# Performance work log

Hardware: AMD Instinct MI355X
Metric: run time of the kernel (lower is better)

## Reference

```python
import jax, jax.numpy as jnp
import numpy as np

N = 100000   # nodes
E = 3200000  # edges (avg degree 32)
F = 10       # input features
H = 20       # hidden dim
G = 512      # graphs in batch
L = 2        # labels


def xavier(key, shape):
    fan_in, fan_out = shape[0], shape[1]
    a = jnp.sqrt(6.0 / (fan_in + fan_out))
    return jax.random.uniform(key, shape, jnp.float32, -a, a)


def setup_inputs() -> dict:
    key = jax.random.key(0)
    ks = jax.random.split(key, 12)
    x = jax.random.normal(ks[0], (N, F), jnp.float32)
    edge_index = jax.random.randint(ks[1], (2, E), 0, N, jnp.int64)
    batch = jnp.sort(jax.random.randint(ks[2], (N,), 0, G, jnp.int64))
    return {
        "x": x,
        "edge_index": edge_index,
        "batch": batch,
        # layer 1: F -> H
        "W_rel1": xavier(ks[3], (F, H)), "b1": jnp.zeros((H,), jnp.float32),
        "W_root1": xavier(ks[4], (F, H)),
        # layer 2: H -> H
        "W_rel2": xavier(ks[5], (H, H)), "b2": jnp.zeros((H,), jnp.float32),
        "W_root2": xavier(ks[6], (H, H)),
        # layer 3: H -> H
        "W_rel3": xavier(ks[7], (H, H)), "b3": jnp.zeros((H,), jnp.float32),
        "W_root3": xavier(ks[8], (H, H)),
        # readout linear: 2H -> L
        "W_lin": xavier(ks[9], (2 * H, L)), "b_lin": jnp.zeros((L,), jnp.float32),
    }


def _graph_conv(x, src, dst, W_rel, b, W_root):
    # PyG GraphConv: out = lin_rel(sum_{j->i} x_j) + lin_root(x_i)
    agg = jax.ops.segment_sum(x[src], dst, num_segments=N)  # [N, d_in]
    return agg @ W_rel + b + x @ W_root


def reference(x, edge_index, batch, W_rel1, b1, W_root1, W_rel2, b2, W_root2,
              W_rel3, b3, W_root3, W_lin, b_lin):
    src, dst = edge_index[0], edge_index[1]
    h = jax.nn.relu(_graph_conv(x, src, dst, W_rel1, b1, W_root1))
    h = jax.nn.relu(_graph_conv(h, src, dst, W_rel2, b2, W_root2))
    h = jax.nn.relu(_graph_conv(h, src, dst, W_rel3, b3, W_root3))  # [N, H]
    # global max / mean pool over graphs
    maxp = jax.ops.segment_max(h, batch, num_segments=G)            # [G, H]
    sump = jax.ops.segment_sum(h, batch, num_segments=G)            # [G, H]
    counts = jax.ops.segment_sum(jnp.ones((h.shape[0], 1), h.dtype), batch,
                                 num_segments=G)                    # [G, 1]
    nonempty = counts > 0
    maxp = jnp.where(nonempty, maxp, 0.0)
    meanp = sump / jnp.maximum(counts, 1.0)
    pooled = jnp.concatenate([maxp, meanp], axis=-1)                # [G, 2H]
    return pooled @ W_lin + b_lin
```

## Files before the change

kernel.cpp:

```cpp
#include <hip/hip_runtime.h>
#include <hip/hip_bf16.h>

#define NN 100000
#define FF 10
#define HH 20
#define GG 512
#define LL 2

#define NB 500
#define BNODES 200
#define CAP 7168
#define HB 100
#define SCAP 3712
#define TILE 4096
#define SRC_BITS 17
#define SRC_MASK 0x1FFFFu

__device__ inline unsigned short f2bf(float f) {
  unsigned u = __float_as_uint(f);
  unsigned r = u + 0x7FFFu + ((u >> 16) & 1u);
  return (unsigned short)(r >> 16);
}
__device__ inline float bflo(unsigned u) { return __uint_as_float(u << 16); }
__device__ inline float bfhi(unsigned u) { return __uint_as_float(u & 0xFFFF0000u); }

__global__ __launch_bounds__(512) void init_kernel(
    float* __restrict__ sump, int* __restrict__ maxp, float* __restrict__ cnt,
    int* __restrict__ cursor) {
  int i = blockIdx.x * 512 + threadIdx.x;
  if (i < GG * HH) {
    sump[i] = 0.0f;
    maxp[i] = 0;
  }
  if (i < GG) cnt[i] = 0.0f;
  if (i < NB) cursor[i] = 0;
}

__global__ __launch_bounds__(512) void multisplit_kernel(
    const int* __restrict__ src, const int* __restrict__ dst,
    int* __restrict__ cursor, unsigned int* __restrict__ pay, int E,
    const float* __restrict__ x, unsigned short* __restrict__ xb, int ncast) {
  __shared__ int lhist[NB];
  __shared__ int lofs[NB];
  __shared__ int gbase[NB];
  __shared__ int lcur[NB];
  __shared__ unsigned int sord[TILE];
  __shared__ unsigned short sdbk[TILE];
  __shared__ int ss[512];
  int t = threadIdx.x;

  {
    int per = (ncast + gridDim.x - 1) / gridDim.x;
    int c0 = blockIdx.x * per;
    int c1 = c0 + per;
    if (c1 > ncast) c1 = ncast;
    for (int i = c0 + t; i < c1; i += 512)
      xb[i] = f2bf(__builtin_nontemporal_load(x + i));
  }

  if (t < NB) lhist[t] = 0;
  __syncthreads();

  int base = blockIdx.x * TILE;
  int count = E - base;
  if (count > TILE) count = TILE;

  for (int i = t; i < count; i += 512)
    atomicAdd(&lhist[dst[base + i] / BNODES], 1);
  __syncthreads();

  int own = (t < NB) ? lhist[t] : 0;
  ss[t] = own;
  __syncthreads();
  for (int off = 1; off < 512; off <<= 1) {
    int a0 = (t >= off) ? ss[t - off] : 0;
    __syncthreads();
    ss[t] += a0;
    __syncthreads();
  }
  if (t < NB) {
    lofs[t] = ss[t] - own;
    int bo = own ? atomicAdd(&cursor[t], own) : 0;
    if (bo > CAP - own) bo = CAP - own;
    gbase[t] = t * CAP + bo;
    lcur[t] = 0;
  }
  __syncthreads();

  for (int i = t; i < count; i += 512) {
    int e = base + i;
    int d = __builtin_nontemporal_load(dst + e);
    int s = __builtin_nontemporal_load(src + e);
    int bk = d / BNODES;
    int ld = d - bk * BNODES;
    int r = atomicAdd(&lcur[bk], 1);
    int slot = lofs[bk] + r;
    sord[slot] = ((unsigned)ld << SRC_BITS) | (unsigned)s;
    sdbk[slot] = (unsigned short)bk;
  }
  __syncthreads();

  for (int i = t; i < count; i += 512) {
    int bk = sdbk[i];
    pay[gbase[bk] + (i - lofs[bk])] = sord[i];
  }
}

__global__ __launch_bounds__(512) void bucket_csr_kernel(
    const unsigned int* __restrict__ pay, const int* __restrict__ cursor,
    int* __restrict__ srt, int* __restrict__ rofs, int* __restrict__ rend) {
  __shared__ int lhist[BNODES];
  __shared__ int lofs[BNODES];
  __shared__ int lcur[BNODES];
  __shared__ int ss[512];
  int b = blockIdx.x;
  int t = threadIdx.x;
  int k0 = b * CAP;
  int ecnt = cursor[b];
  if (ecnt > CAP) ecnt = CAP;

  if (t < BNODES) lhist[t] = 0;
  __syncthreads();
  for (int k = t; k < ecnt; k += 512)
    atomicAdd(&lhist[pay[k0 + k] >> SRC_BITS], 1);
  __syncthreads();

  int own = (t < BNODES) ? lhist[t] : 0;
  ss[t] = own;
  __syncthreads();
  for (int off = 1; off < 512; off <<= 1) {
    int a0 = (t >= off) ? ss[t - off] : 0;
    __syncthreads();
    ss[t] += a0;
    __syncthreads();
  }
  if (t < BNODES) {
    int ex = ss[t] - own;
    lofs[t] = ex;
    lcur[t] = 0;
    rofs[b * BNODES + t] = k0 + ex;
    rend[b * BNODES + t] = k0 + ex + own;
  }
  __syncthreads();

  for (int k = t; k < ecnt; k += 512) {
    unsigned p = pay[k0 + k];
    int ld = p >> SRC_BITS;
    int r = atomicAdd(&lcur[ld], 1);
    srt[k0 + lofs[ld] + r] = (int)(p & SRC_MASK);
  }
}

template<int DIN>
__global__ __launch_bounds__(512) void bucket_layer_kernel(
    const unsigned short* __restrict__ hin, const int* __restrict__ srt,
    const int* __restrict__ rofs, const int* __restrict__ rend,
    const float* __restrict__ Wrel, const float* __restrict__ bias,
    const float* __restrict__ Wroot, unsigned short* __restrict__ hout) {
  constexpr int AST = (DIN == 10) ? 11 : 21;
  constexpr int CH = DIN / 5;
  __shared__ int sSrc[SCAP];
  __shared__ float acc[HB * AST];
  __shared__ unsigned short roots[HB * DIN];
  __shared__ float sWrel[DIN * HH];
  __shared__ float sWroot[DIN * HH];
  __shared__ float sb[HH];
  __shared__ int sRofs[HB];
  __shared__ int sRend[HB];
  __shared__ int sSeg0, sSegLen;
  int b2 = blockIdx.x;
  int t = threadIdx.x;
  int nbase = b2 * HB;

  for (int i = t; i < DIN * HH; i += 512) {
    sWrel[i] = Wrel[i];
    sWroot[i] = Wroot[i];
  }
  if (t < HH) sb[t] = bias[t];
  if (t < HB) {
    sRofs[t] = rofs[nbase + t];
    sRend[t] = rend[nbase + t];
  }
  if (t == 0) {
    int s0 = rofs[nbase];
    int sl = rend[nbase + HB - 1] - s0;
    sSeg0 = s0;
    sSegLen = sl < SCAP ? sl : SCAP;
  }
  {
    const unsigned* rs = (const unsigned*)(hin + (size_t)nbase * DIN);
    unsigned* rd = (unsigned*)roots;
    for (int i = t; i < HB * DIN / 2; i += 512) rd[i] = rs[i];
  }
  __syncthreads();

  int seg0 = sSeg0, seglen = sSegLen;
  for (int i = t; i < seglen; i += 512)
    sSrc[i] = __builtin_nontemporal_load(srt + seg0 + i);
  __syncthreads();

  if (t < HB * 5) {
    int ln = t / 5;
    int c = t - ln * 5;
    int k0 = sRofs[ln] - seg0;
    int k1 = sRend[ln] - seg0;
    if (k1 > seglen) k1 = seglen;
    const unsigned short* xb = hin + c * CH;
    if (CH == 4) {
      float a0 = 0, a1 = 0, a2 = 0, a3 = 0;
      float b0 = 0, b1 = 0, b2 = 0, b3 = 0;
      int k = k0;
      for (; k + 3 < k1; k += 4) {
        int s0 = sSrc[k], s1 = sSrc[k + 1], s2 = sSrc[k + 2], s3 = sSrc[k + 3];
        uint2 u0 = *(const uint2*)(xb + (size_t)s0 * DIN);
        uint2 u1 = *(const uint2*)(xb + (size_t)s1 * DIN);
        uint2 u2 = *(const uint2*)(xb + (size_t)s2 * DIN);
        uint2 u3 = *(const uint2*)(xb + (size_t)s3 * DIN);
        a0 += bflo(u0.x); a1 += bfhi(u0.x); a2 += bflo(u0.y); a3 += bfhi(u0.y);
        b0 += bflo(u1.x); b1 += bfhi(u1.x); b2 += bflo(u1.y); b3 += bfhi(u1.y);
        a0 += bflo(u2.x); a1 += bfhi(u2.x); a2 += bflo(u2.y); a3 += bfhi(u2.y);
        b0 += bflo(u3.x); b1 += bfhi(u3.x); b2 += bflo(u3.y); b3 += bfhi(u3.y);
      }
      for (; k < k1; k++) {
        uint2 u = *(const uint2*)(xb + (size_t)sSrc[k] * DIN);
        a0 += bflo(u.x); a1 += bfhi(u.x); a2 += bflo(u.y); a3 += bfhi(u.y);
      }
      float* a = acc + ln * AST + c * CH;
      a[0] = a0 + b0; a[1] = a1 + b1; a[2] = a2 + b2; a[3] = a3 + b3;
    } else {
      float a0 = 0, a1 = 0;
      float b0 = 0, b1 = 0;
      int k = k0;
      for (; k + 3 < k1; k += 4) {
        int s0 = sSrc[k], s1 = sSrc[k + 1], s2 = sSrc[k + 2], s3 = sSrc[k + 3];
        unsigned u0 = *(const unsigned*)(xb + (size_t)s0 * DIN);
        unsigned u1 = *(const unsigned*)(xb + (size_t)s1 * DIN);
        unsigned u2 = *(const unsigned*)(xb + (size_t)s2 * DIN);
        unsigned u3 = *(const unsigned*)(xb + (size_t)s3 * DIN);
        a0 += bflo(u0); a1 += bfhi(u0);
        b0 += bflo(u1); b1 += bfhi(u1);
        a0 += bflo(u2); a1 += bfhi(u2);
        b0 += bflo(u3); b1 += bfhi(u3);
      }
      for (; k < k1; k++) {
        unsigned u = *(const unsigned*)(xb + (size_t)sSrc[k] * DIN);
        a0 += bflo(u); a1 += bfhi(u);
      }
      float* a = acc + ln * AST + c * CH;
      a[0] = a0 + b0; a[1] = a1 + b1;
    }
  }
  __syncthreads();

  for (int idx = t; idx < HB * HH; idx += 512) {
    int ln = idx / HH;
    int j = idx - ln * HH;
    const float* a = acc + ln * AST;
    const unsigned short* r = roots + ln * DIN;
    float v = sb[j];
#pragma unroll
    for (int f = 0; f < DIN; f++) {
      v += a[f] * sWrel[f * HH + j];
      v += bflo((unsigned)r[f]) * sWroot[f * HH + j];
    }
    hout[(size_t)nbase * HH + idx] = f2bf(fmaxf(v, 0.0f));
  }
}

__global__ __launch_bounds__(512) void bucket_layer_pool_kernel(
    const unsigned short* __restrict__ hin, const int* __restrict__ srt,
    const int* __restrict__ rofs, const int* __restrict__ rend,
    const float* __restrict__ Wrel, const float* __restrict__ bias,
    const float* __restrict__ Wroot, const int* __restrict__ batch,
    float* __restrict__ sump, int* __restrict__ maxp,
    float* __restrict__ cnt) {
  constexpr int DIN = 20;
  constexpr int AST = 21;
  __shared__ int sSrc[SCAP];
  __shared__ float acc[HB * AST];
  __shared__ unsigned short roots[HB * DIN];
  __shared__ int sBatch[HB];
  __shared__ float sWrel[DIN * HH];
  __shared__ float sWroot[DIN * HH];
  __shared__ float sb[HH];
  __shared__ int sRofs[HB];
  __shared__ int sRend[HB];
  __shared__ int sSeg0, sSegLen;
  int b2 = blockIdx.x;
  int t = threadIdx.x;
  int nbase = b2 * HB;

  for (int i = t; i < DIN * HH; i += 512) {
    sWrel[i] = Wrel[i];
    sWroot[i] = Wroot[i];
  }
  if (t < HH) sb[t] = bias[t];
  if (t < HB) {
    sRofs[t] = rofs[nbase + t];
    sRend[t] = rend[nbase + t];
    sBatch[t] = batch[nbase + t];
  }
  if (t == 0) {
    int s0 = rofs[nbase];
    int sl = rend[nbase + HB - 1] - s0;
    sSeg0 = s0;
    sSegLen = sl < SCAP ? sl : SCAP;
  }
  {
    const unsigned* rs = (const unsigned*)(hin + (size_t)nbase * DIN);
    unsigned* rd = (unsigned*)roots;
    for (int i = t; i < HB * DIN / 2; i += 512) rd[i] = rs[i];
  }
  __syncthreads();

  int seg0 = sSeg0, seglen = sSegLen;
  for (int i = t; i < seglen; i += 512)
    sSrc[i] = __builtin_nontemporal_load(srt + seg0 + i);
  __syncthreads();

  if (t < HB * 5) {
    int ln = t / 5;
    int c = t - ln * 5;
    int k0 = sRofs[ln] - seg0;
    int k1 = sRend[ln] - seg0;
    if (k1 > seglen) k1 = seglen;
    const unsigned short* xb = hin + c * 4;
    float a0 = 0, a1 = 0, a2 = 0, a3 = 0;
    float b0 = 0, b1 = 0, b2 = 0, b3 = 0;
    int k = k0;
    for (; k + 3 < k1; k += 4) {
      int s0 = sSrc[k], s1 = sSrc[k + 1], s2 = sSrc[k + 2], s3 = sSrc[k + 3];
      uint2 u0 = *(const uint2*)(xb + (size_t)s0 * 20);
      uint2 u1 = *(const uint2*)(xb + (size_t)s1 * 20);
      uint2 u2 = *(const uint2*)(xb + (size_t)s2 * 20);
      uint2 u3 = *(const uint2*)(xb + (size_t)s3 * 20);
      a0 += bflo(u0.x); a1 += bfhi(u0.x); a2 += bflo(u0.y); a3 += bfhi(u0.y);
      b0 += bflo(u1.x); b1 += bfhi(u1.x); b2 += bflo(u1.y); b3 += bfhi(u1.y);
      a0 += bflo(u2.x); a1 += bfhi(u2.x); a2 += bflo(u2.y); a3 += bfhi(u2.y);
      b0 += bflo(u3.x); b1 += bfhi(u3.x); b2 += bflo(u3.y); b3 += bfhi(u3.y);
    }
    for (; k < k1; k++) {
      uint2 u = *(const uint2*)(xb + (size_t)sSrc[k] * 20);
      a0 += bflo(u.x); a1 += bfhi(u.x); a2 += bflo(u.y); a3 += bfhi(u.y);
    }
    float* a = acc + ln * AST + c * 4;
    a[0] = a0 + b0; a[1] = a1 + b1; a[2] = a2 + b2; a[3] = a3 + b3;
  }
  __syncthreads();

  float vreg[4];
#pragma unroll
  for (int u = 0; u < 4; u++) {
    int idx = t + u * 512;
    if (idx < HB * HH) {
      int ln = idx / HH;
      int j = idx - ln * HH;
      const float* a = acc + ln * AST;
      const unsigned short* r = roots + ln * DIN;
      float v = sb[j];
#pragma unroll
      for (int f = 0; f < DIN; f++) {
        v += a[f] * sWrel[f * HH + j];
        v += bflo((unsigned)r[f]) * sWroot[f * HH + j];
      }
      vreg[u] = fmaxf(v, 0.0f);
    }
  }
  __syncthreads();
#pragma unroll
  for (int u = 0; u < 4; u++) {
    int idx = t + u * 512;
    if (idx < HB * HH) {
      int ln = idx / HH;
      int j = idx - ln * HH;
      acc[ln * AST + j] = vreg[u];
    }
  }
  __syncthreads();

  int g0 = sBatch[0];
  int g1 = sBatch[HB - 1];
  int ngr = g1 - g0 + 1;
  for (int it = t; it < ngr * HH; it += 512) {
    int gi = it / HH;
    int j = it - gi * HH;
    int g = g0 + gi;
    float s = 0.0f, m = 0.0f;
    int c = 0;
    for (int ln = 0; ln < HB; ln++) {
      if (sBatch[ln] == g) {
        float v = acc[ln * AST + j];
        s += v;
        m = fmaxf(m, v);
        c++;
      }
    }
    if (c) {
      atomicAdd(&sump[g * HH + j], s);
      atomicMax(&maxp[g * HH + j], __float_as_int(m));
      if (j == 0) atomicAdd(&cnt[g], (float)c);
    }
  }
}

__global__ __launch_bounds__(256) void readout_kernel(
    const float* __restrict__ sump, const int* __restrict__ maxp,
    const float* __restrict__ cnt, const float* __restrict__ Wlin,
    const float* __restrict__ blin, float* __restrict__ out) {
  int idx = blockIdx.x * 256 + threadIdx.x;
  if (idx >= GG * LL) return;
  int g = idx / LL;
  int l = idx - g * LL;
  float c = cnt[g];
  float inv = 1.0f / fmaxf(c, 1.0f);
  float acc = blin[l];
#pragma unroll
  for (int j = 0; j < HH; j++) {
    float mx = __int_as_float(maxp[g * HH + j]);
    float mean = sump[g * HH + j] * inv;
    acc += mx * Wlin[j * LL + l];
    acc += mean * Wlin[(HH + j) * LL + l];
  }
  out[idx] = acc;
}

extern "C" void kernel_launch(void* const* d_in, const int* in_sizes, int n_in,
                              void* d_out, int out_size, void* d_ws,
                              size_t ws_size, hipStream_t stream) {
  const float* x = (const float*)d_in[0];
  const int* edge_index = (const int*)d_in[1];
  const int* batch = (const int*)d_in[2];
  const float* W_rel1 = (const float*)d_in[3];
  const float* b1 = (const float*)d_in[4];
  const float* W_root1 = (const float*)d_in[5];
  const float* W_rel2 = (const float*)d_in[6];
  const float* b2 = (const float*)d_in[7];
  const float* W_root2 = (const float*)d_in[8];
  const float* W_rel3 = (const float*)d_in[9];
  const float* b3 = (const float*)d_in[10];
  const float* W_root3 = (const float*)d_in[11];
  const float* W_lin = (const float*)d_in[12];
  const float* b_lin = (const float*)d_in[13];
  float* out = (float*)d_out;

  const int E = in_sizes[1] / 2;
  const int n_nodes = in_sizes[0] / FF;
  const int* src = edge_index;
  const int* dst = edge_index + E;

  unsigned int* pay = (unsigned int*)d_ws;
  int* srt = (int*)(pay + (size_t)NB * CAP);
  int* rofs = srt + (size_t)NB * CAP;
  int* rend = rofs + NN;
  int* cursor = rend + NN;
  float* sump = (float*)(cursor + 512);
  int* maxp = (int*)(sump + GG * HH);
  float* cnt = (float*)(maxp + GG * HH);
  unsigned short* xb = (unsigned short*)(cnt + 512);
  unsigned short* h1 = xb + (size_t)NN * FF;
  unsigned short* h2 = h1 + (size_t)NN * HH;

  const int edge_tiles = (E + TILE - 1) / TILE;

  init_kernel<<<(GG * HH + 511) / 512, 512, 0, stream>>>(
      sump, maxp, cnt, cursor);

  multisplit_kernel<<<edge_tiles, 512, 0, stream>>>(
      src, dst, cursor, pay, E, x, xb, n_nodes * FF);
  bucket_csr_kernel<<<NB, 512, 0, stream>>>(pay, cursor, srt, rofs, rend);

  bucket_layer_kernel<FF><<<NB * 2, 512, 0, stream>>>(
      xb, srt, rofs, rend, W_rel1, b1, W_root1, h1);
  bucket_layer_kernel<HH><<<NB * 2, 512, 0, stream>>>(
      h1, srt, rofs, rend, W_rel2, b2, W_root2, h2);
  bucket_layer_pool_kernel<<<NB * 2, 512, 0, stream>>>(
      h2, srt, rofs, rend, W_rel3, b3, W_root3, batch, sump, maxp, cnt);

  readout_kernel<<<(GG * LL + 255) / 256, 256, 0, stream>>>(
      sump, maxp, cnt, W_lin, b_lin, out);
}
```

Measured before the change: 249.8 us.

## Fuse bucket CSR construction into the layer-1 graph conv kernel

Merges the per-bucket CSR sort kernel with the first GraphConv layer. Each of the two half-blocks per bucket redoes the histogram, scan and scatter, keeps its own slice of sorted sources in shared memory, and aggregates layer 1 straight from it. Only half 0 writes srt, rofs and rend for the later layers. This removes one launch and the global re-read of srt for layer 1, but duplicates the sorting work across the two halves and raises shared memory use per block.

Result: slower. 258.1 us (+3.3%).

```diff
diff --git a/kernel.cpp b/kernel.cpp
--- a/kernel.cpp
+++ b/kernel.cpp
@@ -106,23 +106,49 @@
   }
 }
 
-__global__ __launch_bounds__(512) void bucket_csr_kernel(
-    const unsigned int* __restrict__ pay, const int* __restrict__ cursor,
-    int* __restrict__ srt, int* __restrict__ rofs, int* __restrict__ rend) {
+__global__ __launch_bounds__(512) void layer1_csr_kernel(
+    const unsigned short* __restrict__ xb, const unsigned int* __restrict__ pay,
+    const int* __restrict__ cursor,
+    int* __restrict__ srt, int* __restrict__ rofs, int* __restrict__ rend,
+    const float* __restrict__ Wrel, const float* __restrict__ bias,
+    const float* __restrict__ Wroot, unsigned short* __restrict__ hout) {
+  constexpr int DIN = 10;
+  constexpr int AST = 11;
   __shared__ int lhist[BNODES];
-  __shared__ int lofs[BNODES];
+  __shared__ int lofsb[BNODES];
   __shared__ int lcur[BNODES];
   __shared__ int ss[512];
-  int b = blockIdx.x;
+  __shared__ int sSrc[SCAP];
+  __shared__ float acc[HB * AST];
+  __shared__ unsigned short roots[HB * DIN];
+  __shared__ float sWrel[DIN * HH];
+  __shared__ float sWroot[DIN * HH];
+  __shared__ float sb[HH];
+  __shared__ int sSegBase, sSegLen;
+  int b2 = blockIdx.x;
+  int bk = b2 >> 1;
+  int half = b2 & 1;
   int t = threadIdx.x;
-  int k0 = b * CAP;
-  int ecnt = cursor[b];
+  int nbase = b2 * HB;
+  int k0g = bk * CAP;
+  int ecnt = cursor[bk];
   if (ecnt > CAP) ecnt = CAP;
 
+  for (int i = t; i < DIN * HH; i += 512) {
+    sWrel[i] = Wrel[i];
+    sWroot[i] = Wroot[i];
+  }
+  if (t < HH) sb[t] = bias[t];
+  {
+    const unsigned* rs = (const unsigned*)(xb + (size_t)nbase * DIN);
+    unsigned* rd = (unsigned*)roots;
+    for (int i = t; i < HB * DIN / 2; i += 512) rd[i] = rs[i];
+  }
+
   if (t < BNODES) lhist[t] = 0;
   __syncthreads();
   for (int k = t; k < ecnt; k += 512)
-    atomicAdd(&lhist[pay[k0 + k] >> SRC_BITS], 1);
+    atomicAdd(&lhist[pay[k0g + k] >> SRC_BITS], 1);
   __syncthreads();
 
   int own = (t < BNODES) ? lhist[t] : 0;
@@ -135,19 +161,80 @@
     __syncthreads();
   }
   if (t < BNODES) {
-    int ex = ss[t] - own;
-    lofs[t] = ex;
+    lofsb[t] = ss[t] - own;
     lcur[t] = 0;
-    rofs[b * BNODES + t] = k0 + ex;
-    rend[b * BNODES + t] = k0 + ex + own;
-  }
-  __syncthreads();
+    if (half == 0) {
+      rofs[bk * BNODES + t] = k0g + ss[t] - own;
+      rend[bk * BNODES + t] = k0g + ss[t];
+    }
+  }
+  __syncthreads();
+  if (t == 0) {
+    int n0 = half * HB;
+    int sbv = lofsb[n0];
+    int sev = lofsb[n0 + HB - 1] + lhist[n0 + HB - 1];
+    sSegBase = sbv;
+    int sl = sev - sbv;
+    sSegLen = sl < SCAP ? sl : SCAP;
+  }
+  __syncthreads();
+  int segBase = sSegBase, segLen = sSegLen;
 
   for (int k = t; k < ecnt; k += 512) {
-    unsigned p = pay[k0 + k];
+    unsigned p = pay[k0g + k];
     int ld = p >> SRC_BITS;
+    int s = (int)(p & SRC_MASK);
     int r = atomicAdd(&lcur[ld], 1);
-    srt[k0 + lofs[ld] + r] = (int)(p & SRC_MASK);
+    int pos = lofsb[ld] + r;
+    if (half == 0) srt[k0g + pos] = s;
+    int rel = pos - segBase;
+    if (rel >= 0 && rel < segLen) sSrc[rel] = s;
+  }
+  __syncthreads();
+
+  if (t < HB * 5) {
+    int ln = t / 5;
+    int c = t - ln * 5;
+    int lnode = half * HB + ln;
+    int k0 = lofsb[lnode] - segBase;
+    int k1 = k0 + lhist[lnode];
+    if (k1 > segLen) k1 = segLen;
+    const unsigned short* xp = xb + c * 2;
+    float a0 = 0, a1 = 0;
+    float b0 = 0, b1 = 0;
+    int k = k0;
+    for (; k + 3 < k1; k += 4) {
+      int s0 = sSrc[k], s1 = sSrc[k + 1], s2 = sSrc[k + 2], s3 = sSrc[k + 3];
+      unsigned u0 = *(const unsigned*)(xp + (size_t)s0 * DIN);
+      unsigned u1 = *(const unsigned*)(xp + (size_t)s1 * DIN);
+      unsigned u2 = *(const unsigned*)(xp + (size_t)s2 * DIN);
+      unsigned u3 = *(const unsigned*)(xp + (size_t)s3 * DIN);
+      a0 += bflo(u0); a1 += bfhi(u0);
+      b0 += bflo(u1); b1 += bfhi(u1);
+      a0 += bflo(u2); a1 += bfhi(u2);
+      b0 += bflo(u3); b1 += bfhi(u3);
+    }
+    for (; k < k1 && k >= 0; k++) {
+      unsigned u = *(const unsigned*)(xp + (size_t)sSrc[k] * DIN);
+      a0 += bflo(u); a1 += bfhi(u);
+    }
+    float* a = acc + ln * AST + c * 2;
+    a[0] = a0 + b0; a[1] = a1 + b1;
+  }
+  __syncthreads();
+
+  for (int idx = t; idx < HB * HH; idx += 512) {
+    int ln = idx / HH;
+    int j = idx - ln * HH;
+    const float* a = acc + ln * AST;
+    const unsigned short* r = roots + ln * DIN;
+    float v = sb[j];
+#pragma unroll
+    for (int f = 0; f < DIN; f++) {
+      v += a[f] * sWrel[f * HH + j];
+      v += bflo((unsigned)r[f]) * sWroot[f * HH + j];
+    }
+    hout[(size_t)nbase * HH + idx] = f2bf(fmaxf(v, 0.0f));
   }
 }
 
@@ -467,10 +554,10 @@
 
   multisplit_kernel<<<edge_tiles, 512, 0, stream>>>(
       src, dst, cursor, pay, E, x, xb, n_nodes * FF);
-  bucket_csr_kernel<<<NB, 512, 0, stream>>>(pay, cursor, srt, rofs, rend);
-
-  bucket_layer_kernel<FF><<<NB * 2, 512, 0, stream>>>(
-      xb, srt, rofs, rend, W_rel1, b1, W_root1, h1);
+
+  layer1_csr_kernel<<<NB * 2, 512, 0, stream>>>(
+      xb, pay, cursor, srt, rofs, rend, W_rel1, b1, W_root1, h1);
+
   bucket_layer_kernel<HH><<<NB * 2, 512, 0, stream>>>(
       h1, srt, rofs, rend, W_rel2, b2, W_root2, h2);
   bucket_layer_pool_kernel<<<NB * 2, 512, 0, stream>>>(
```
